# Optimization experiments

Measured on AMD Instinct MI355X. Metric: run time of the kernel, lower is better.

## Reference

```python
import jax, jax.numpy as jnp
import numpy as np

N_NODES = 8192
D_FEAT = 128
R_BITS = 8      # rows per band
B_BANDS = 64    # number of LSH bands
D_THRESH = 0.25 # cosine-distance threshold from LSH(z, d=0.25, ...)


def setup_inputs() -> dict:
    key = jax.random.key(0)
    k1, k2, k3 = jax.random.split(key, 3)
    z = jax.random.normal(k1, (N_NODES, D_FEAT), dtype=jnp.float32)
    # random hyperplanes for signed-projection LSH: r*b = 512 planes
    H = jax.random.normal(k2, (D_FEAT, R_BITS * B_BANDS), dtype=jnp.float32)
    edge_index = jax.random.randint(k3, (2, N_NODES * 16), 0, N_NODES, dtype=jnp.int64)
    return {"z": z, "H": H, "edge_index": edge_index}


def reference(z, H, edge_index):
    # edge_index is unused by forward_all (kept for signature fidelity).
    N = z.shape[0]
    # --- hyperplane LSH signatures ---
    bits = (z @ H) > 0                              # [N, r*b] bool
    bits = bits.reshape(N, B_BANDS, R_BITS)         # [N, b, r]
    powers = (2 ** jnp.arange(R_BITS)).astype(jnp.int32)
    codes = jnp.sum(bits.astype(jnp.int32) * powers, axis=-1)  # [N, b] band hash codes

    # --- candidate pairs: collide in at least one band (OR over bands) ---
    def band_or(mask, c):  # c: [N] codes for one band
        return mask | (c[:, None] == c[None, :]), None
    collide, _ = jax.lax.scan(band_or, jnp.zeros((N, N), dtype=bool), codes.T)

    # --- exact cosine similarity on candidates ---
    zn = z / jnp.linalg.norm(z, axis=1, keepdims=True)
    S = zn @ zn.T                                   # [N, N] cosine similarity
    dist = 1.0 - S                                  # cosine distance

    eye = jnp.eye(N, dtype=bool)
    # pairs kept by LSH: colliding, within distance threshold, off-diagonal
    keep = collide & (dist < D_THRESH) & (~eye)
    # adjacency[v1, v2] = 1 - dist = cos_sim (sigmoid=True path); identity on diagonal
    A = jnp.where(keep, S, 0.0) + eye.astype(S.dtype)
    return A
```

## Files before the change

### kernel.cpp

```cpp
#include <hip/hip_runtime.h>
#include <hip/hip_bf16.h>

#define N_NODES 8192
#define D_FEAT 128

typedef __bf16 bf16x8 __attribute__((ext_vector_type(8)));
typedef float f32x4 __attribute__((ext_vector_type(4)));

__device__ __forceinline__ void lgkm_barrier() {
  asm volatile("s_waitcnt lgkmcnt(0)\n\ts_barrier" ::: "memory");
}
__device__ __forceinline__ void lgkm_fence() {
  asm volatile("s_waitcnt lgkmcnt(0)" ::: "memory");
}

__device__ __attribute__((noinline)) bool lsh_collide(
    const float* __restrict__ z, const float* __restrict__ H, int i, int j) {
  for (int b = 0; b < 64; ++b) {
    unsigned ci = 0, cj = 0;
    for (int bit = 0; bit < 8; ++bit) {
      int col = b * 8 + bit;
      float di = 0.f, dj = 0.f;
      for (int k = 0; k < D_FEAT; ++k) {
        float h = H[(size_t)k * 512 + col];
        di += z[(size_t)i * D_FEAT + k] * h;
        dj += z[(size_t)j * D_FEAT + k] * h;
      }
      if (di > 0.f) ci |= (1u << bit);
      if (dj > 0.f) cj |= (1u << bit);
    }
    if (ci == cj) return true;
  }
  return false;
}

__device__ __forceinline__ unsigned pack_bf16x2(float x, float y) {
  __hip_bfloat16 bx = __float2bfloat16(x), by = __float2bfloat16(y);
  return (unsigned)(*(unsigned short*)&bx) |
         ((unsigned)(*(unsigned short*)&by) << 16);
}

__device__ __forceinline__ void stage_tile(const float* __restrict__ z, int blk,
                                           unsigned short (*T)[128], int tid) {
  int row = tid >> 1, half = tid & 1;
  const float4* src = (const float4*)(z + (size_t)(blk * 128 + row) * D_FEAT + half * 64);
  float4 v[16];
#pragma unroll
  for (int c = 0; c < 16; ++c) v[c] = src[c];
  float ss = 0.f;
#pragma unroll
  for (int c = 0; c < 16; ++c)
    ss += v[c].x * v[c].x + v[c].y * v[c].y + v[c].z * v[c].z + v[c].w * v[c].w;
  ss += __shfl_xor(ss, 1);
  float inv = rsqrtf(ss);
#pragma unroll
  for (int c = 0; c < 8; ++c) {
    float4 a = v[2 * c], b = v[2 * c + 1];
    uint4 o;
    o.x = pack_bf16x2(a.x * inv, a.y * inv);
    o.y = pack_bf16x2(a.z * inv, a.w * inv);
    o.z = pack_bf16x2(b.x * inv, b.y * inv);
    o.w = pack_bf16x2(b.z * inv, b.w * inv);
    ((uint4*)&T[row][0])[(half * 8 + c) ^ (row & 15)] = o;
  }
}

__global__ __launch_bounds__(256, 2) void sim_kernel(const float* __restrict__ z,
                                                     const float* __restrict__ H,
                                                     float* __restrict__ out) {
  __shared__ __align__(16) unsigned char smem_raw[65536];
  unsigned short (*As)[128] = (unsigned short (*)[128])smem_raw;
  unsigned short (*Bs)[128] = (unsigned short (*)[128])(smem_raw + 32768);
  float* fS = (float*)smem_raw;

  int tid = threadIdx.x;
  int b = (int)blockIdx.x;
  int bm0 = b & 7;
  int bn = b >> 3;

  int wv = tid >> 6, lane = tid & 63;
  int wm = (wv >> 1) * 64, wn = (wv & 1) * 64;
  int m16 = lane & 15, g = lane >> 4;
  float* fSw = fS + wv * 2048;

  stage_tile(z, bn, Bs, tid);

  for (int t = 0; t < 8; ++t) {
    int bm = bm0 * 8 + t;

    lgkm_barrier();
    stage_tile(z, bm, As, tid);
    lgkm_barrier();

    f32x4 acc[4][4] = {};
#pragma unroll
    for (int kc = 0; kc < 4; ++kc) {
      bf16x8 fa[4], fb[4];
      int chunk = kc * 4 + g;
      int cs = (chunk ^ m16) * 8;
#pragma unroll
      for (int tt = 0; tt < 4; ++tt) {
        fa[tt] = *(const bf16x8*)&As[wm + tt * 16 + m16][cs];
        fb[tt] = *(const bf16x8*)&Bs[wn + tt * 16 + m16][cs];
      }
#pragma unroll
      for (int tm = 0; tm < 4; ++tm)
#pragma unroll
        for (int tn = 0; tn < 4; ++tn)
          acc[tm][tn] = __builtin_amdgcn_mfma_f32_16x16x32_bf16(fa[tm], fb[tn], acc[tm][tn], 0, 0, 0);
    }

    lgkm_barrier();

#pragma unroll
    for (int tm = 0; tm < 4; ++tm) {
      float* slab = fSw + (tm & 1) * 1024;
#pragma unroll
      for (int tn = 0; tn < 4; ++tn) {
        int colq = tn * 16 + m16;
        int j = bn * 128 + wn + colq;
        f32x4 c = acc[tm][tn];
#pragma unroll
        for (int r = 0; r < 4; ++r) {
          int rs = g * 4 + r;
          int i = bm * 128 + wm + tm * 16 + rs;
          float s = c[r];
          float val = 0.0f;
          if (i == j) {
            val = 1.0f;
          } else if (s > 0.75f) {
            if (lsh_collide(z, H, i, j)) val = s;
          }
          slab[rs * 64 + (((colq >> 2) ^ rs) << 2) + (colq & 3)] = val;
        }
      }
      lgkm_fence();
#pragma unroll
      for (int it = 0; it < 4; ++it) {
        int rs = it * 4 + g;
        f32x4 v = *(const f32x4*)&slab[rs * 64 + ((m16 ^ rs) << 2)];
        int grow = bm * 128 + wm + tm * 16 + rs;
        *(f32x4*)&out[(size_t)grow * N_NODES + bn * 128 + wn + m16 * 4] = v;
      }
    }
  }
}

extern "C" void kernel_launch(void* const* d_in, const int* in_sizes, int n_in,
                              void* d_out, int out_size, void* d_ws, size_t ws_size,
                              hipStream_t stream) {
  const float* z = (const float*)d_in[0];
  const float* H = (const float*)d_in[1];
  float* out = (float*)d_out;
  (void)d_ws; (void)ws_size;

  sim_kernel<<<512, 256, 0, stream>>>(z, H, out);
}
```

Measured before the change: 277.7 us.

## Precompute normalized bf16 tiles and double-buffer A tiles via async LDS loads

Moves row normalization and bf16 conversion into a separate pre-pass kernel that writes pre-swizzled tiles to workspace. The main kernel then streams A tiles straight into LDS with global_load_lds, double-buffered so the next tile's load overlaps the current MFMA work. B fragments are held in registers for the whole block. This removes the normalization repeated in every block and the load stalls on the critical path, at the cost of an extra launch, more register pressure from 16 held fragments, and epilogue scratch that now shares a buffer with the staged tiles.

```diff
diff --git a/kernel.cpp b/kernel.cpp
--- a/kernel.cpp
+++ b/kernel.cpp
@@ -10,8 +10,20 @@
 __device__ __forceinline__ void lgkm_barrier() {
   asm volatile("s_waitcnt lgkmcnt(0)\n\ts_barrier" ::: "memory");
 }
+__device__ __forceinline__ void stage_barrier() {
+  asm volatile("s_waitcnt vmcnt(16) lgkmcnt(0)\n\ts_barrier" ::: "memory");
+}
+__device__ __forceinline__ void vm0_barrier() {
+  asm volatile("s_waitcnt vmcnt(0) lgkmcnt(0)\n\ts_barrier" ::: "memory");
+}
 __device__ __forceinline__ void lgkm_fence() {
   asm volatile("s_waitcnt lgkmcnt(0)" ::: "memory");
+}
+
+__device__ __forceinline__ void async_copy16(void* lds, const void* g) {
+  __builtin_amdgcn_global_load_lds(
+      (const __attribute__((address_space(1))) void*)g,
+      (__attribute__((address_space(3))) void*)lds, 16, 0, 0);
 }
 
 __device__ __attribute__((noinline)) bool lsh_collide(
@@ -40,10 +52,11 @@
          ((unsigned)(*(unsigned short*)&by) << 16);
 }
 
-__device__ __forceinline__ void stage_tile(const float* __restrict__ z, int blk,
-                                           unsigned short (*T)[128], int tid) {
-  int row = tid >> 1, half = tid & 1;
-  const float4* src = (const float4*)(z + (size_t)(blk * 128 + row) * D_FEAT + half * 64);
+__global__ __launch_bounds__(256) void norm_kernel(const float* __restrict__ z,
+                                                   uint4* __restrict__ zn) {
+  int gt = (int)blockIdx.x * 256 + (int)threadIdx.x;
+  int row = gt >> 1, half = gt & 1;
+  const float4* src = (const float4*)(z + (size_t)row * D_FEAT + half * 64);
   float4 v[16];
 #pragma unroll
   for (int c = 0; c < 16; ++c) v[c] = src[c];
@@ -53,6 +66,8 @@
     ss += v[c].x * v[c].x + v[c].y * v[c].y + v[c].z * v[c].z + v[c].w * v[c].w;
   ss += __shfl_xor(ss, 1);
   float inv = rsqrtf(ss);
+  int blk = row >> 7, r = row & 127;
+  uint4* dst = zn + (size_t)blk * 2048 + r * 16;
 #pragma unroll
   for (int c = 0; c < 8; ++c) {
     float4 a = v[2 * c], b = v[2 * c + 1];
@@ -61,17 +76,15 @@
     o.y = pack_bf16x2(a.z * inv, a.w * inv);
     o.z = pack_bf16x2(b.x * inv, b.y * inv);
     o.w = pack_bf16x2(b.z * inv, b.w * inv);
-    ((uint4*)&T[row][0])[(half * 8 + c) ^ (row & 15)] = o;
+    dst[(half * 8 + c) ^ (r & 15)] = o;
   }
 }
 
 __global__ __launch_bounds__(256, 2) void sim_kernel(const float* __restrict__ z,
                                                      const float* __restrict__ H,
+                                                     const uint4* __restrict__ zn,
                                                      float* __restrict__ out) {
-  __shared__ __align__(16) unsigned char smem_raw[65536];
-  unsigned short (*As)[128] = (unsigned short (*)[128])smem_raw;
-  unsigned short (*Bs)[128] = (unsigned short (*)[128])(smem_raw + 32768);
-  float* fS = (float*)smem_raw;
+  __shared__ __align__(16) unsigned char smem[65536];
 
   int tid = threadIdx.x;
   int b = (int)blockIdx.x;
@@ -81,33 +94,61 @@
   int wv = tid >> 6, lane = tid & 63;
   int wm = (wv >> 1) * 64, wn = (wv & 1) * 64;
   int m16 = lane & 15, g = lane >> 4;
-  float* fSw = fS + wv * 2048;
-
-  stage_tile(z, bn, Bs, tid);
+
+  {
+    const uint4* gB = zn + (size_t)bn * 2048;
+    const uint4* gA = zn + (size_t)(bm0 * 8) * 2048;
+#pragma unroll
+    for (int i = 0; i < 8; ++i) {
+      int c = i * 256 + tid;
+      async_copy16(smem + 32768 + c * 16, gB + c);
+      async_copy16(smem + c * 16, gA + c);
+    }
+  }
+  vm0_barrier();
+
+  bf16x8 fbr[16];
+  {
+    unsigned short (*Bs)[128] = (unsigned short (*)[128])(smem + 32768);
+#pragma unroll
+    for (int kc = 0; kc < 4; ++kc) {
+      int cs = ((kc * 4 + g) ^ m16) * 8;
+#pragma unroll
+      for (int tt = 0; tt < 4; ++tt)
+        fbr[kc * 4 + tt] = *(const bf16x8*)&Bs[wn + tt * 16 + m16][cs];
+    }
+  }
 
   for (int t = 0; t < 8; ++t) {
     int bm = bm0 * 8 + t;
-
-    lgkm_barrier();
-    stage_tile(z, bm, As, tid);
-    lgkm_barrier();
+    unsigned short (*As)[128] = (unsigned short (*)[128])(smem + (t & 1) * 32768);
+    float* fSw = (float*)(smem + (t & 1) * 32768) + wv * 2048;
+
+    stage_barrier();
+
+    if (t < 7) {
+      const uint4* gA = zn + (size_t)(bm + 1) * 2048;
+      unsigned char* dstbuf = smem + ((t + 1) & 1) * 32768;
+#pragma unroll
+      for (int i = 0; i < 8; ++i) {
+        int c = i * 256 + tid;
+        async_copy16(dstbuf + c * 16, gA + c);
+      }
+    }
 
     f32x4 acc[4][4] = {};
 #pragma unroll
     for (int kc = 0; kc < 4; ++kc) {
-      bf16x8 fa[4], fb[4];
-      int chunk = kc * 4 + g;
-      int cs = (chunk ^ m16) * 8;
-#pragma unroll
-      for (int tt = 0; tt < 4; ++tt) {
+      bf16x8 fa[4];
+      int cs = ((kc * 4 + g) ^ m16) * 8;
+#pragma unroll
+      for (int tt = 0; tt < 4; ++tt)
         fa[tt] = *(const bf16x8*)&As[wm + tt * 16 + m16][cs];
-        fb[tt] = *(const bf16x8*)&Bs[wn + tt * 16 + m16][cs];
-      }
 #pragma unroll
       for (int tm = 0; tm < 4; ++tm)
 #pragma unroll
         for (int tn = 0; tn < 4; ++tn)
-          acc[tm][tn] = __builtin_amdgcn_mfma_f32_16x16x32_bf16(fa[tm], fb[tn], acc[tm][tn], 0, 0, 0);
+          acc[tm][tn] = __builtin_amdgcn_mfma_f32_16x16x32_bf16(fa[tm], fbr[kc * 4 + tn], acc[tm][tn], 0, 0, 0);
     }
 
     lgkm_barrier();
@@ -152,7 +193,9 @@
   const float* z = (const float*)d_in[0];
   const float* H = (const float*)d_in[1];
   float* out = (float*)d_out;
-  (void)d_ws; (void)ws_size;
-
-  sim_kernel<<<512, 256, 0, stream>>>(z, H, out);
-}
+  uint4* zn = (uint4*)d_ws;
+  (void)ws_size;
+
+  norm_kernel<<<64, 256, 0, stream>>>(z, zn);
+  sim_kernel<<<512, 256, 0, stream>>>(z, H, zn, out);
+}
```

After: 337.0 us. 21.3% more time.
